# Optimization experiments

Hardware: AMD Instinct MI355X
Metric: run time of the kernel (lower is better)

Reference implementation:

```python
import jax, jax.numpy as jnp
import numpy as np
from jax.ops import segment_sum, segment_max

H, C = 2, 32            # heads, per-head channels (hidden = H*C = 64)
HID = H * C
L = 2                   # num_layers
EPS = 1e-5              # LayerNorm eps
NEG_SLOPE = 0.2         # GATv2 leaky_relu slope
NP_, NA_, E_, DIN, DOUT = 200_000, 100_000, 1_000_000, 128, 64


def setup_inputs() -> dict:
    ks = jax.random.split(jax.random.key(0), 16)
    s = 0.05
    return {
        "x_paper": jax.random.normal(ks[0], (NP_, DIN), jnp.float32),
        "x_author": jax.random.normal(ks[1], (NA_, DIN), jnp.float32),
        "ei_writes_src": jax.random.randint(ks[2], (E_,), 0, NA_),
        "ei_writes_dst": jax.random.randint(ks[3], (E_,), 0, NP_),
        "ei_rev_src": jax.random.randint(ks[4], (E_,), 0, NP_),
        "ei_rev_dst": jax.random.randint(ks[5], (E_,), 0, NA_),
        "ei_cites_src": jax.random.randint(ks[6], (E_,), 0, NP_),
        "ei_cites_dst": jax.random.randint(ks[7], (E_,), 0, NP_),
        "inW_paper": jax.random.normal(ks[8], (DIN, HID)) * s,
        "inW_author": jax.random.normal(ks[9], (DIN, HID)) * s,
        "gat_Wl": jax.random.normal(ks[10], (L, 3, HID, HID)) * s,
        "gat_bl": jnp.zeros((L, 3, HID)),
        "gat_Wr": jax.random.normal(ks[11], (L, 3, HID, HID)) * s,
        "gat_br": jnp.zeros((L, 3, HID)),
        "gat_att": jax.random.normal(ks[12], (L, 3, H, C)) * s,
        "gat_bias": jnp.zeros((L, 3, HID)),
        "ln_scale": jnp.ones((L, 2, HID)),
        "ln_bias": jnp.zeros((L, 2, HID)),
        "outW_paper": jax.random.normal(ks[13], (HID, DOUT)) * s,
        "outb_paper": jnp.zeros((DOUT,)),
        "outW_author": jax.random.normal(ks[14], (HID, DOUT)) * s,
        "outb_author": jnp.zeros((DOUT,)),
    }


def _gatv2(h_src, h_dst, src, dst, Wl, bl, Wr, br, att, bias):
    """PyG GATv2Conv(64, 32, heads=2, concat=True, add_self_loops=False)."""
    nd = h_dst.shape[0]
    xl = (h_src @ Wl + bl).reshape(-1, H, C)           # [Ns,H,C]
    xr = (h_dst @ Wr + br).reshape(-1, H, C)           # [Nd,H,C]
    e = jax.nn.leaky_relu(xl[src] + xr[dst], NEG_SLOPE)  # [E,H,C] gather+add
    logits = jnp.einsum('ehc,hc->eh', e, att)          # [E,H]
    m = jax.lax.stop_gradient(segment_max(logits, dst, num_segments=nd))
    ex = jnp.exp(logits - m[dst])                      # stable segment softmax
    den = segment_sum(ex, dst, num_segments=nd)
    alpha = ex / den[dst]                              # [E,H]
    agg = segment_sum(xl[src] * alpha[..., None], dst, num_segments=nd)
    return agg.reshape(nd, HID) + bias


def _ln(v, g, b):
    mu = v.mean(-1, keepdims=True)
    var = ((v - mu) ** 2).mean(-1, keepdims=True)
    return (v - mu) / jnp.sqrt(var + EPS) * g + b


def _forward(x_paper, x_author, ints, params):
    ws, wd, rs, rd, cs, cd = ints
    (inW_p, inW_a, Wl, bl, Wr, br, att, gbias, lng, lnb,
     oWp, obp, oWa, oba) = params
    h = {"paper": x_paper @ inW_p, "author": x_author @ inW_a}
    rels = [("author", "paper", ws, wd),   # writes
            ("paper", "author", rs, rd),   # rev_writes
            ("paper", "paper", cs, cd)]    # cites
    for l in range(L):
        new = {"paper": 0.0, "author": 0.0}
        for r, (st, dt, src, dst) in enumerate(rels):
            new[dt] = new[dt] + _gatv2(h[st], h[dt], src, dst,
                                       Wl[l, r], bl[l, r], Wr[l, r], br[l, r],
                                       att[l, r], gbias[l, r])
        # HeteroConv(aggr='sum') -> LayerNorm -> ReLU (dropout is eval no-op)
        h = {nt: jax.nn.relu(_ln(new[nt], lng[l, i], lnb[l, i]))
             for i, nt in enumerate(("paper", "author"))}
    out_p = h["paper"] @ oWp + obp
    out_a = h["author"] @ oWa + oba
    return jnp.concatenate([out_p, out_a], axis=0)  # [Np+Na, DOUT]


def reference(x_paper, x_author, ei_writes_src, ei_writes_dst, ei_rev_src,
              ei_rev_dst, ei_cites_src, ei_cites_dst, inW_paper, inW_author,
              gat_Wl, gat_bl, gat_Wr, gat_br, gat_att, gat_bias, ln_scale,
              ln_bias, outW_paper, outb_paper, outW_author, outb_author):
    ints = (ei_writes_src, ei_writes_dst, ei_rev_src, ei_rev_dst,
            ei_cites_src, ei_cites_dst)
    params = (inW_paper, inW_author, gat_Wl, gat_bl, gat_Wr, gat_br, gat_att,
              gat_bias, ln_scale, ln_bias, outW_paper, outb_paper,
              outW_author, outb_author)
    return _forward(x_paper, x_author, ints, params)
```

## Files before the change

### kernel.cpp

```cpp
#include <hip/hip_runtime.h>
#include <hip/hip_bf16.h>


#define NPAPER  200000
#define NAUTHOR 100000
#define NEDGE   1000000

#define NB128_P 1563
#define NB128_A 782

#define BIN_SHIFT 10
#define BIN_SIZE  1024
#define NBIN_P    196
#define NBIN_A    98
#define NBIN_TOT  (NBIN_P + NBIN_A + NBIN_P)
#define CAP_P     8192
#define CAP_A     16384
#define RELOFF1   (NBIN_P * CAP_P)
#define RELOFF2   (NBIN_P * CAP_P + NBIN_A * CAP_A)
#define BINNED_TOT (NBIN_P * CAP_P + NBIN_A * CAP_A + NBIN_P * CAP_P)
#define EPT       8
#define NBLK_BIN  489

#define LOG2E 1.4426950408889634f

typedef __attribute__((ext_vector_type(8))) short short8;
typedef __attribute__((ext_vector_type(4))) float f32x4;
typedef __attribute__((ext_vector_type(2))) float f32x2;

__device__ inline float b2f(__hip_bfloat16 v) { return __bfloat162float(v); }

__device__ inline short f2bs(float f) {
    unsigned u = __float_as_uint(f);
    u += 0x7FFFu + ((u >> 16) & 1u);
    return (short)(u >> 16);
}

__device__ inline float wireF(const void* p, int i, int f32) {
    return f32 ? ((const float*)p)[i]
               : b2f(((const __hip_bfloat16*)p)[i]);
}

__device__ inline const int* sel3(int r, const int* a, const int* b, const int* c) {
    return r == 0 ? a : (r == 1 ? b : c);
}
__device__ inline int* sel3m(int r, int* a, int* b, int* c) {
    return r == 0 ? a : (r == 1 ? b : c);
}

__device__ inline f32x2 unpack2(unsigned u) {
    f32x2 r;
    r.x = __uint_as_float(u << 16);
    r.y = __uint_as_float(u & 0xFFFF0000u);
    return r;
}

template <int CTRL>
__device__ inline float dpp_add(float v) {
    const int r = __builtin_amdgcn_update_dpp(
        0, __float_as_int(v), CTRL, 0xF, 0xF, true);
    return v + __int_as_float(r);
}
__device__ inline float hs16(float v) {
    v = dpp_add<0x128>(v);
    v = dpp_add<0x124>(v);
    v = dpp_add<0x122>(v);
    v = dpp_add<0x121>(v);
    return v;
}
__device__ inline float sum32(float v) {
    v = hs16(v);
    const int s = __builtin_amdgcn_ds_swizzle(__float_as_int(v), 0x401F);
    return v + __int_as_float(s);
}

__global__ void detect_mode(const unsigned* __restrict__ lns, int* __restrict__ flag) {
    if (threadIdx.x == 0 && blockIdx.x == 0)
        flag[0] = (lns[0] == 0x3F800000u) ? 1 : 0;
}

template <int K, int OUT_MODE, bool A_WIRE, bool DBUF>
__global__ __launch_bounds__(256) void gemm_ps(
    const void* __restrict__ A0v, const void* __restrict__ B0v, int b0_off,
    const void* __restrict__ bias0v, int bias0_off,
    void* __restrict__ Y0v, int N0, int row0_off, int nt0, int g0,
    const void* __restrict__ A1v, const void* __restrict__ B1v, int b1_off,
    const void* __restrict__ bias1v, int bias1_off,
    void* __restrict__ Y1v, int N1, int row1_off, int nt1,
    const int* __restrict__ flagp)
{
    const int f32 = flagp[0];
    constexpr int SB = K + 8;
    constexpr int OUTB = (OUT_MODE == 2) ? 8192 : 4096;
    __shared__ short Bs[64 * SB];
    __shared__ float sbias[64];
    __shared__ __align__(16) char outs[4][OUTB];

    int bid = blockIdx.x;
    const void* Av; const void* Bv; int b_off; const void* biasv; int bias_off;
    void* Yv; int N; int row_off; int ntiles; int gstep; int t0;
    if (bid < g0) {
        Av = A0v; Bv = B0v; b_off = b0_off; biasv = bias0v; bias_off = bias0_off;
        Yv = Y0v; N = N0; row_off = row0_off; ntiles = nt0; gstep = g0; t0 = bid;
    } else {
        Av = A1v; Bv = B1v; b_off = b1_off; biasv = bias1v; bias_off = bias1_off;
        Yv = Y1v; N = N1; row_off = row1_off; ntiles = nt1;
        gstep = (int)gridDim.x - g0; t0 = bid - g0;
    }

    const int tid = threadIdx.x;
    for (int idx = tid; idx < K * 64; idx += 256) {
        const int k = idx >> 6;
        const int n = idx & 63;
        const short v = f32 ? f2bs(((const float*)Bv)[b_off + idx])
                            : ((const short*)Bv)[b_off + idx];
        Bs[n * SB + k] = v;
    }
    if (tid < 64)
        sbias[tid] = biasv ? wireF(biasv, bias_off + tid, f32) : 0.0f;
    __syncthreads();

    if (t0 >= ntiles) return;

    const int wave = tid >> 6;
    const int lane = tid & 63;
    const int l15  = lane & 15;
    const int quad = lane >> 4;
    char* const myout = outs[wave];

    short8 a_cur[K / 32][2], a_nxt[K / 32][2];

    auto ldA = [&](int t, short8 (&af)[K / 32][2]) {
        const int rowb = t * 128 + wave * 32;
#pragma unroll
        for (int kit = 0; kit < K / 32; kit++) {
            const int k0 = kit * 32 + quad * 8;
#pragma unroll
            for (int rg = 0; rg < 2; rg++) {
                int r = rowb + rg * 16 + l15;
                if (r >= N) r = N - 1;
                if (A_WIRE && f32) {
                    const float* Ar = (const float*)Av + (size_t)r * K + k0;
                    const float4 x0 = *reinterpret_cast<const float4*>(Ar);
                    const float4 x1 = *reinterpret_cast<const float4*>(Ar + 4);
                    short8 tt;
                    tt[0] = f2bs(x0.x); tt[1] = f2bs(x0.y);
                    tt[2] = f2bs(x0.z); tt[3] = f2bs(x0.w);
                    tt[4] = f2bs(x1.x); tt[5] = f2bs(x1.y);
                    tt[6] = f2bs(x1.z); tt[7] = f2bs(x1.w);
                    af[kit][rg] = tt;
                } else {
                    af[kit][rg] = *reinterpret_cast<const short8*>(
                        (const short*)Av + (size_t)r * K + k0);
                }
            }
        }
    };

    if (DBUF) ldA(t0, a_cur);
    for (int t = t0; ; ) {
        const int tn = t + gstep;
        const bool hn = tn < ntiles;
        if (DBUF) {
            if (hn) ldA(tn, a_nxt);
        } else {
            ldA(t, a_cur);
        }

        f32x4 acc[2][4] = {};
#pragma unroll
        for (int kit = 0; kit < K / 32; kit++) {
            const int k0 = kit * 32 + quad * 8;
#pragma unroll
            for (int cg = 0; cg < 4; cg++) {
                const short8 bf = *reinterpret_cast<const short8*>(
                    &Bs[(cg * 16 + l15) * SB + k0]);
#pragma unroll
                for (int rg = 0; rg < 2; rg++)
                    acc[rg][cg] = __builtin_amdgcn_mfma_f32_16x16x32_bf16(
                        a_cur[kit][rg], bf, acc[rg][cg], 0, 0, 0);
            }
        }

        const int rowbase = t * 128 + wave * 32;
        const bool bf16out = (OUT_MODE == 0) || !f32;
        if (bf16out) {
#pragma unroll
            for (int rg = 0; rg < 2; rg++)
#pragma unroll
            for (int cg = 0; cg < 4; cg++) {
                const int col = cg * 16 + l15;
                const float bv = sbias[col];
#pragma unroll
                for (int r = 0; r < 4; r++) {
                    const int rl = rg * 16 + quad * 4 + r;
                    const unsigned a = (unsigned)(rl * 128 + col * 2)
                                     ^ (unsigned)((rl & 7) << 4);
                    *reinterpret_cast<short*>(myout + a) =
                        f2bs(acc[rg][cg][r] + bv);
                }
            }
#pragma unroll
            for (int i = 0; i < 4; i++) {
                const unsigned a = i * 1024 + lane * 16;
                const int rl = a >> 7;
                const unsigned as = a ^ (unsigned)((rl & 7) << 4);
                const int grow = rowbase + rl;
                if (grow < N) {
                    const uint4 v = *reinterpret_cast<const uint4*>(myout + as);
                    *reinterpret_cast<uint4*>(
                        (__hip_bfloat16*)Yv
                        + (size_t)(grow + row_off) * 64 + ((a & 127) >> 1)) = v;
                }
            }
        } else {
#pragma unroll
            for (int rg = 0; rg < 2; rg++)
#pragma unroll
            for (int cg = 0; cg < 4; cg++) {
                const int col = cg * 16 + l15;
                const float bv = sbias[col];
#pragma unroll
                for (int r = 0; r < 4; r++) {
                    const int rl = rg * 16 + quad * 4 + r;
                    const unsigned a = (unsigned)(rl * 256 + col * 4)
                                     ^ (unsigned)((rl & 15) << 4);
                    *reinterpret_cast<float*>(myout + a) = acc[rg][cg][r] + bv;
                }
            }
#pragma unroll
            for (int i = 0; i < 8; i++) {
                const unsigned a = i * 1024 + lane * 16;
                const int rl = a >> 8;
                const unsigned as = a ^ (unsigned)((rl & 15) << 4);
                const int grow = rowbase + rl;
                if (grow < N) {
                    const float4 v = *reinterpret_cast<const float4*>(myout + as);
                    *reinterpret_cast<float4*>(
                        (float*)Yv
                        + (size_t)(grow + row_off) * 64 + ((a & 255) >> 2)) = v;
                }
            }
        }

        if (!hn) break;
        if (DBUF) {
#pragma unroll
            for (int kit = 0; kit < K / 32; kit++) {
                a_cur[kit][0] = a_nxt[kit][0];
                a_cur[kit][1] = a_nxt[kit][1];
            }
        }
        t = tn;
    }
}

__global__ __launch_bounds__(256) void scatter_pad(
    const int* __restrict__ s0, const int* __restrict__ s1, const int* __restrict__ s2,
    const int* __restrict__ d0, const int* __restrict__ d1, const int* __restrict__ d2,
    int* __restrict__ g_bincnt, unsigned* __restrict__ binned)
{
    int bid = blockIdx.x;
    const int rel = bid / NBLK_BIN;
    bid -= rel * NBLK_BIN;
    const int* src = sel3(rel, s0, s1, s2);
    const int* dst = sel3(rel, d0, d1, d2);
    const int nbin = (rel == 1) ? NBIN_A : NBIN_P;
    const int cap  = (rel == 1) ? CAP_A : CAP_P;
    const int boff = (rel == 0) ? 0 : ((rel == 1) ? NBIN_P : NBIN_P + NBIN_A);
    unsigned* bout = binned + ((rel == 0) ? 0 : ((rel == 1) ? RELOFF1 : RELOFF2));

    __shared__ int lcnt[NBIN_P];
    __shared__ int lbase[NBIN_P];
    for (int i = threadIdx.x; i < nbin; i += 256) lcnt[i] = 0;
    __syncthreads();

    const int e0 = bid * (256 * EPT) + threadIdx.x;
    int mybin[EPT], myslot[EPT];
    unsigned mypack[EPT];
#pragma unroll
    for (int i = 0; i < EPT; i++) {
        const int e = e0 + i * 256;
        if (e < NEDGE) {
            const int D = dst[e];
            const int b = D >> BIN_SHIFT;
            mybin[i]  = b;
            mypack[i] = (unsigned)src[e] | ((unsigned)(D & (BIN_SIZE - 1)) << 18);
            myslot[i] = atomicAdd(&lcnt[b], 1);
        } else mybin[i] = -1;
    }
    __syncthreads();
    for (int i = threadIdx.x; i < nbin; i += 256) {
        const int cn = lcnt[i];
        lbase[i] = cn ? atomicAdd(&g_bincnt[boff + i], cn) : 0;
    }
    __syncthreads();
#pragma unroll
    for (int i = 0; i < EPT; i++)
        if (mybin[i] >= 0) {
            const int pos = lbase[mybin[i]] + myslot[i];
            if (pos < cap)
                bout[(size_t)mybin[i] * cap + pos] = mypack[i];
        }
}

__global__ __launch_bounds__(256) void csr_binscan(
    const int* __restrict__ g_bincnt, int* __restrict__ g_binbase,
    int* __restrict__ rp0, int* __restrict__ rp1, int* __restrict__ rp2)
{
    __shared__ int lds[NBIN_TOT];
    for (int i = threadIdx.x; i < NBIN_TOT; i += 256) lds[i] = g_bincnt[i];
    __syncthreads();
    if (threadIdx.x < 3) {
        const int rel  = threadIdx.x;
        const int nbin = (rel == 1) ? NBIN_A : NBIN_P;
        const int boff = (rel == 0) ? 0 : ((rel == 1) ? NBIN_P : NBIN_P + NBIN_A);
        int run = 0;
        for (int i = 0; i < nbin; i++) {
            const int cn = lds[boff + i];
            lds[boff + i] = run;
            run += cn;
        }
        int* rp = sel3m(rel, rp0, rp1, rp2);
        rp[(rel == 1) ? NAUTHOR : NPAPER] = NEDGE;
    }
    __syncthreads();
    for (int i = threadIdx.x; i < NBIN_TOT; i += 256)
        g_binbase[i] = lds[i];
}

__global__ __launch_bounds__(256) void csr_build(
    const unsigned* __restrict__ binned, const int* __restrict__ g_binbase,
    const int* __restrict__ g_bincnt,
    int* __restrict__ rp0, int* __restrict__ rp1, int* __restrict__ rp2,
    int* __restrict__ c0, int* __restrict__ c1, int* __restrict__ c2)
{
    int bid = blockIdx.x;
    int rel, boff, N, cap;
    const unsigned* bin;
    if (bid < NBIN_P) {
        rel = 0; boff = 0; N = NPAPER; cap = CAP_P;
        bin = binned + (size_t)bid * CAP_P;
    } else if (bid < NBIN_P + NBIN_A) {
        rel = 1; bid -= NBIN_P; boff = NBIN_P; N = NAUTHOR; cap = CAP_A;
        bin = binned + RELOFF1 + (size_t)bid * CAP_A;
    } else {
        rel = 2; bid -= NBIN_P + NBIN_A; boff = NBIN_P + NBIN_A; N = NPAPER; cap = CAP_P;
        bin = binned + RELOFF2 + (size_t)bid * CAP_P;
    }

    const int base = g_binbase[boff + bid];
    int cnt = g_bincnt[boff + bid];
    if (cnt > cap) cnt = cap;
    int* row_ptr = sel3m(rel, rp0, rp1, rp2);
    int* csr     = sel3m(rel, c0, c1, c2);

    __shared__ int off[BIN_SIZE];
    __shared__ int lds[256];
    for (int i = threadIdx.x; i < BIN_SIZE; i += 256) off[i] = 0;
    __syncthreads();
    for (int i = threadIdx.x; i < cnt; i += 256)
        atomicAdd(&off[bin[i] >> 18], 1);
    __syncthreads();

    const int t  = threadIdx.x;
    const int i4 = t * 4;
    const int v0 = off[i4], v1 = off[i4 + 1], v2 = off[i4 + 2], v3 = off[i4 + 3];
    const int tsum = v0 + v1 + v2 + v3;
    lds[t] = tsum;
    __syncthreads();
    for (int o = 1; o < 256; o <<= 1) {
        const int x = (t >= o) ? lds[t - o] : 0;
        __syncthreads();
        lds[t] += x;
        __syncthreads();
    }
    const int run = lds[t] - tsum;
    const int ex0 = run, ex1 = ex0 + v0, ex2 = ex1 + v1, ex3 = ex2 + v2;
    off[i4] = ex0; off[i4 + 1] = ex1; off[i4 + 2] = ex2; off[i4 + 3] = ex3;
    const int d0g = bid * BIN_SIZE + i4;
    if (d0g     < N) row_ptr[d0g]     = base + ex0;
    if (d0g + 1 < N) row_ptr[d0g + 1] = base + ex1;
    if (d0g + 2 < N) row_ptr[d0g + 2] = base + ex2;
    if (d0g + 3 < N) row_ptr[d0g + 3] = base + ex3;
    __syncthreads();

    for (int i = threadIdx.x; i < cnt; i += 256) {
        const unsigned pk = bin[i];
        const int slot = atomicAdd(&off[pk >> 18], 1);
        csr[base + slot] = (int)(pk & 0x3FFFFu);
    }
}

__device__ inline void gat_core_h(
    const int* __restrict__ csr_src, const unsigned* __restrict__ xlw,
    int beg, int end, int hbase, int cp,
    const f32x2 xr2, float a0, float a1,
    float& accx, float& accy, float& den)
{
    const int n = end - beg;
    const int m = (n + 3) >> 2;
    f32x2 acc2 = {0.0f, 0.0f};
    float dn = 0.0f;

    int lidx;
    {
        const int e = beg + cp;
        lidx = csr_src[(e < end) ? e : beg];
    }
    auto loadq = [&](unsigned (&B)[4], int it) {
#pragma unroll
        for (int k = 0; k < 4; k++) {
            const int s = __shfl(lidx, hbase + ((it & 7) << 2) + k, 64);
            B[k] = xlw[(size_t)s * 32 + cp];
        }
    };

    unsigned G[4];
    loadq(G, 0);
    for (int it = 0; ; ) {
        const int nx = it + 1;
        const bool hn = nx < m;
        unsigned H[4];
        if (hn) {
            if ((nx & 7) == 0) {
                const int e = beg + (nx << 2) + cp;
                lidx = csr_src[(e < end) ? e : beg];
            }
            loadq(H, nx);
        }

        f32x2 xv[4];
        float u[4];
#pragma unroll
        for (int k = 0; k < 4; k++) {
            xv[k] = unpack2(G[k]);
            f32x2 t = xv[k] + xr2;
            t = __builtin_elementwise_max(t, 0.2f * t);
            u[k] = fmaf(t.y, a1, t.x * a0);
        }
#pragma unroll
        for (int k = 0; k < 4; k++) u[k] = hs16(u[k]);
#pragma unroll
        for (int k = 0; k < 4; k++) {
            const float e = ((it << 2) + k < n)
                          ? __builtin_amdgcn_exp2f(u[k]) : 0.0f;
            acc2 += e * xv[k];
            dn   += e;
        }

        if (!hn) break;
        G[0] = H[0]; G[1] = H[1]; G[2] = H[2]; G[3] = H[3];
        it = nx;
    }
    accx = acc2.x;
    accy = acc2.y;
    den  = dn;
}

__global__ __launch_bounds__(256) void gat_all(
    const int* __restrict__ rp0, const int* __restrict__ cs0,
    const __hip_bfloat16* __restrict__ xl0, const __hip_bfloat16* __restrict__ xr0,
    const int* __restrict__ rp2, const int* __restrict__ cs2,
    const __hip_bfloat16* __restrict__ xl2, const __hip_bfloat16* __restrict__ xr2,
    const int* __restrict__ rp1, const int* __restrict__ cs1,
    const __hip_bfloat16* __restrict__ xl1, const __hip_bfloat16* __restrict__ xr1,
    const void* __restrict__ att, int ao0, int ao1, int ao2,
    const void* __restrict__ gb, int bo0, int bo1, int bo2,
    const void* __restrict__ lng, int goffP, int goffA,
    const void* __restrict__ lnb, int boffP, int boffA,
    __hip_bfloat16* __restrict__ h_p, __hip_bfloat16* __restrict__ h_a,
    const int* __restrict__ flagp)
{
    const int gnode = blockIdx.x * 8 + (threadIdx.x >> 5);
    const int hbase = threadIdx.x & 32;
    const int cp    = threadIdx.x & 31;
    const int f32   = flagp[0];
    const int c0 = 2 * cp, c1 = 2 * cp + 1;

    float vx, vy;
    const void* lg; const void* lb; int goff, boff;
    __hip_bfloat16* hout; int dout;

    if (gnode < NPAPER) {
        const int d = gnode;
        vx = wireF(gb, bo0 + c0, f32) + wireF(gb, bo2 + c0, f32);
        vy = wireF(gb, bo0 + c1, f32) + wireF(gb, bo2 + c1, f32);

        {
            const int beg = rp0[d], end = rp0[d + 1];
            if (beg != end) {
                const unsigned uxr = ((const unsigned*)xr0)[(size_t)d * 32 + cp];
                float ax, ay, dn;
                gat_core_h(cs0, (const unsigned*)xl0, beg, end, hbase, cp,
                           unpack2(uxr),
                           wireF(att, ao0 + c0, f32) * LOG2E,
                           wireF(att, ao0 + c1, f32) * LOG2E, ax, ay, dn);
                vx += ax / dn; vy += ay / dn;
            }
        }
        {
            const int beg = rp2[d], end = rp2[d + 1];
            if (beg != end) {
                const unsigned uxr = ((const unsigned*)xr2)[(size_t)d * 32 + cp];
                float ax, ay, dn;
                gat_core_h(cs2, (const unsigned*)xl2, beg, end, hbase, cp,
                           unpack2(uxr),
                           wireF(att, ao2 + c0, f32) * LOG2E,
                           wireF(att, ao2 + c1, f32) * LOG2E, ax, ay, dn);
                vx += ax / dn; vy += ay / dn;
            }
        }
        lg = lng; lb = lnb; goff = goffP; boff = boffP;
        hout = h_p; dout = d;
    } else {
        const int d = gnode - NPAPER;
        if (d >= NAUTHOR) return;
        vx = wireF(gb, bo1 + c0, f32);
        vy = wireF(gb, bo1 + c1, f32);

        const int beg = rp1[d], end = rp1[d + 1];
        if (beg != end) {
            const unsigned uxr = ((const unsigned*)xr1)[(size_t)d * 32 + cp];
            float ax, ay, dn;
            gat_core_h(cs1, (const unsigned*)xl1, beg, end, hbase, cp,
                       unpack2(uxr),
                       wireF(att, ao1 + c0, f32) * LOG2E,
                       wireF(att, ao1 + c1, f32) * LOG2E, ax, ay, dn);
            vx += ax / dn; vy += ay / dn;
        }
        lg = lng; lb = lnb; goff = goffA; boff = boffA;
        hout = h_a; dout = d;
    }

    const float mu = sum32(vx + vy) * (1.0f / 64.0f);
    const float dx = vx - mu, dy = vy - mu;
    const float var = sum32(dx * dx + dy * dy) * (1.0f / 64.0f);
    const float sc = rsqrtf(var + 1e-5f);
    float y0 = dx * sc * wireF(lg, goff + c0, f32) + wireF(lb, boff + c0, f32);
    float y1 = dy * sc * wireF(lg, goff + c1, f32) + wireF(lb, boff + c1, f32);
    y0 = (y0 < 0.0f) ? 0.0f : y0;
    y1 = (y1 < 0.0f) ? 0.0f : y1;

    const unsigned u = (unsigned)(unsigned short)f2bs(y0)
                     | ((unsigned)(unsigned short)f2bs(y1) << 16);
    ((unsigned*)hout)[(size_t)dout * 32 + cp] = u;
}

extern "C" void kernel_launch(void* const* d_in, const int* in_sizes, int n_in,
                              void* d_out, int out_size, void* d_ws, size_t ws_size,
                              hipStream_t stream)
{
    const void* x_p   = d_in[0];
    const void* x_a   = d_in[1];
    const int* e_ws_s = (const int*)d_in[2];
    const int* e_ws_d = (const int*)d_in[3];
    const int* e_rv_s = (const int*)d_in[4];
    const int* e_rv_d = (const int*)d_in[5];
    const int* e_ci_s = (const int*)d_in[6];
    const int* e_ci_d = (const int*)d_in[7];
    const void* inW_p = d_in[8];
    const void* inW_a = d_in[9];
    const void* Wl    = d_in[10];
    const void* bl    = d_in[11];
    const void* Wr    = d_in[12];
    const void* br    = d_in[13];
    const void* att   = d_in[14];
    const void* gbias = d_in[15];
    const void* lng   = d_in[16];
    const void* lnb   = d_in[17];
    const void* oWp   = d_in[18];
    const void* obp   = d_in[19];
    const void* oWa   = d_in[20];
    const void* oba   = d_in[21];

    char* p = (char*)d_ws;
    auto carve = [&](size_t bytes) -> char* {
        char* r = p;
        p += (bytes + 255) & ~(size_t)255;
        return r;
    };
    int* flag = (int*)carve(256);
    __hip_bfloat16* h_p = (__hip_bfloat16*)carve((size_t)NPAPER  * 64 * 2);
    __hip_bfloat16* h_a = (__hip_bfloat16*)carve((size_t)NAUTHOR * 64 * 2);
    __hip_bfloat16* xl0 = (__hip_bfloat16*)carve((size_t)NAUTHOR * 64 * 2);
    __hip_bfloat16* xr0 = (__hip_bfloat16*)carve((size_t)NPAPER  * 64 * 2);
    __hip_bfloat16* xl1 = (__hip_bfloat16*)carve((size_t)NPAPER  * 64 * 2);
    __hip_bfloat16* xr1 = (__hip_bfloat16*)carve((size_t)NAUTHOR * 64 * 2);
    __hip_bfloat16* xl2 = (__hip_bfloat16*)carve((size_t)NPAPER  * 64 * 2);
    __hip_bfloat16* xr2 = (__hip_bfloat16*)carve((size_t)NPAPER  * 64 * 2);
    int *csr_src[3], *row_ptr[3];
    for (int r = 0; r < 3; r++) {
        csr_src[r] = (int*)carve((size_t)NEDGE * 4);
        row_ptr[r] = (int*)carve(((size_t)NPAPER + 1) * 4);
    }
    unsigned* binned = (unsigned*)carve((size_t)BINNED_TOT * 4);
    int* g_bincnt  = (int*)carve(NBIN_TOT * 4);
    int* g_binbase = (int*)carve(NBIN_TOT * 4);

    detect_mode<<<dim3(1), dim3(64), 0, stream>>>((const unsigned*)lng, flag);

    (void)hipMemsetAsync(g_bincnt, 0, NBIN_TOT * 4, stream);
    scatter_pad<<<dim3(3 * NBLK_BIN), dim3(256), 0, stream>>>(
        e_ws_s, e_rv_s, e_ci_s, e_ws_d, e_rv_d, e_ci_d, g_bincnt, binned);
    csr_binscan<<<dim3(1), dim3(256), 0, stream>>>(
        g_bincnt, g_binbase, row_ptr[0], row_ptr[1], row_ptr[2]);
    csr_build<<<dim3(NBIN_TOT), dim3(256), 0, stream>>>(
        binned, g_binbase, g_bincnt, row_ptr[0], row_ptr[1], row_ptr[2],
        csr_src[0], csr_src[1], csr_src[2]);

    auto gsplit = [](int GT, int nt0, int nt1) -> int {
        int g0 = (int)((long long)GT * nt0 / (nt0 + nt1));
        if (g0 < 1) g0 = 1;
        if (g0 > GT - 1) g0 = GT - 1;
        return g0;
    };

    {
        const int GT = 1024;
        const int g0 = gsplit(GT, NB128_P, NB128_A);
        gemm_ps<128, 0, true, false><<<dim3(GT), dim3(256), 0, stream>>>(
            x_p, inW_p, 0, nullptr, 0, h_p, NPAPER, 0, NB128_P, g0,
            x_a, inW_a, 0, nullptr, 0, h_a, NAUTHOR, 0, NB128_A, flag);
    }

    for (int l = 0; l < 2; l++) {
        const int wo0 = (l * 3 + 0) * 4096, bo0 = (l * 3 + 0) * 64;
        const int wo1 = (l * 3 + 1) * 4096, bo1 = (l * 3 + 1) * 64;
        const int wo2 = (l * 3 + 2) * 4096, bo2 = (l * 3 + 2) * 64;
        const int GT = 1536;

        {
            const int g0 = gsplit(GT, NB128_A, NB128_P);
            gemm_ps<64, 0, false, true><<<dim3(GT), dim3(256), 0, stream>>>(
                h_a, Wl, wo0, bl, bo0, xl0, NAUTHOR, 0, NB128_A, g0,
                h_p, Wr, wo0, br, bo0, xr0, NPAPER, 0, NB128_P, flag);
        }
        {
            const int g0 = gsplit(GT, NB128_P, NB128_P);
            gemm_ps<64, 0, false, true><<<dim3(GT), dim3(256), 0, stream>>>(
                h_p, Wl, wo2, bl, bo2, xl2, NPAPER, 0, NB128_P, g0,
                h_p, Wr, wo2, br, bo2, xr2, NPAPER, 0, NB128_P, flag);
        }
        {
            const int g0 = gsplit(GT, NB128_P, NB128_A);
            gemm_ps<64, 0, false, true><<<dim3(GT), dim3(256), 0, stream>>>(
                h_p, Wl, wo1, bl, bo1, xl1, NPAPER, 0, NB128_P, g0,
                h_a, Wr, wo1, br, bo1, xr1, NAUTHOR, 0, NB128_A, flag);
        }

        gat_all<<<dim3((NPAPER + NAUTHOR) / 8), dim3(256), 0, stream>>>(
            row_ptr[0], csr_src[0], xl0, xr0,
            row_ptr[2], csr_src[2], xl2, xr2,
            row_ptr[1], csr_src[1], xl1, xr1,
            att, bo0, bo1, bo2,
            gbias, bo0, bo1, bo2,
            lng, (l * 2 + 0) * 64, (l * 2 + 1) * 64,
            lnb, (l * 2 + 0) * 64, (l * 2 + 1) * 64,
            h_p, h_a, flag);
    }

    {
        const int GT = 768;
        const int g0 = gsplit(GT, NB128_P, NB128_A);
        gemm_ps<64, 2, false, true><<<dim3(GT), dim3(256), 0, stream>>>(
            h_p, oWp, 0, obp, 0, d_out, NPAPER, 0, NB128_P, g0,
            h_a, oWa, 0, oba, 0, d_out, NAUTHOR, NPAPER, NB128_A, flag);
    }
}
```

Before: 788.7 us.

## Merge per-layer projection GEMMs into one six-job launch; specialize input/output GEMMs

Replaces the three two-job projection GEMM launches per layer with a single launch that covers all six Wl/Wr projections. A block picks its job from a boundary table passed in a struct. The input projection becomes a dedicated kernel with 64-row tiles, no LDS staging and direct scalar bf16 stores, launched on a larger grid. The output GEMM becomes its own specialized kernel. The aim is to cut launch count and tail effects, at the cost of scalar uncoalesced stores in the input GEMM and a per-block job lookup.

```diff
diff --git a/kernel.cpp b/kernel.cpp
--- a/kernel.cpp
+++ b/kernel.cpp
@@ -8,6 +8,8 @@
 
 #define NB128_P 1563
 #define NB128_A 782
+#define NB64_P  3125
+#define NB64_A  1563
 
 #define BIN_SHIFT 10
 #define BIN_SIZE  1024
@@ -79,47 +81,140 @@
         flag[0] = (lns[0] == 0x3F800000u) ? 1 : 0;
 }
 
-template <int K, int OUT_MODE, bool A_WIRE, bool DBUF>
-__global__ __launch_bounds__(256) void gemm_ps(
-    const void* __restrict__ A0v, const void* __restrict__ B0v, int b0_off,
-    const void* __restrict__ bias0v, int bias0_off,
-    void* __restrict__ Y0v, int N0, int row0_off, int nt0, int g0,
-    const void* __restrict__ A1v, const void* __restrict__ B1v, int b1_off,
-    const void* __restrict__ bias1v, int bias1_off,
-    void* __restrict__ Y1v, int N1, int row1_off, int nt1,
+__global__ __launch_bounds__(256) void gemm_in(
+    const void* __restrict__ A0v, const void* __restrict__ B0v,
+    void* __restrict__ Y0v, int N0, int nt0, int g0,
+    const void* __restrict__ A1v, const void* __restrict__ B1v,
+    void* __restrict__ Y1v, int N1, int nt1,
     const int* __restrict__ flagp)
 {
     const int f32 = flagp[0];
-    constexpr int SB = K + 8;
-    constexpr int OUTB = (OUT_MODE == 2) ? 8192 : 4096;
+    constexpr int K = 128, SB = K + 8;
+    __shared__ short Bs[64 * SB];
+
+    int bid = blockIdx.x;
+    const void* Av; const void* Bv; void* Yv; int N, ntiles, gstep, t0;
+    if (bid < g0) {
+        Av = A0v; Bv = B0v; Yv = Y0v; N = N0; ntiles = nt0; gstep = g0; t0 = bid;
+    } else {
+        Av = A1v; Bv = B1v; Yv = Y1v; N = N1; ntiles = nt1;
+        gstep = (int)gridDim.x - g0; t0 = bid - g0;
+    }
+
+    const int tid = threadIdx.x;
+    for (int idx = tid; idx < K * 64; idx += 256) {
+        const int k = idx >> 6, n = idx & 63;
+        const short v = f32 ? f2bs(((const float*)Bv)[idx])
+                            : ((const short*)Bv)[idx];
+        Bs[n * SB + k] = v;
+    }
+    __syncthreads();
+    if (t0 >= ntiles) return;
+
+    const int wave = tid >> 6;
+    const int lane = tid & 63;
+    const int l15  = lane & 15;
+    const int quad = lane >> 4;
+
+    for (int t = t0; t < ntiles; t += gstep) {
+        const int rowbase = t * 64 + wave * 16;
+        int r = rowbase + l15;
+        if (r >= N) r = N - 1;
+
+        short8 af[4];
+#pragma unroll
+        for (int kit = 0; kit < 4; kit++) {
+            const int k0 = kit * 32 + quad * 8;
+            if (f32) {
+                const float* Ar = (const float*)Av + (size_t)r * K + k0;
+                const float4 x0 = *reinterpret_cast<const float4*>(Ar);
+                const float4 x1 = *reinterpret_cast<const float4*>(Ar + 4);
+                short8 tt;
+                tt[0] = f2bs(x0.x); tt[1] = f2bs(x0.y);
+                tt[2] = f2bs(x0.z); tt[3] = f2bs(x0.w);
+                tt[4] = f2bs(x1.x); tt[5] = f2bs(x1.y);
+                tt[6] = f2bs(x1.z); tt[7] = f2bs(x1.w);
+                af[kit] = tt;
+            } else {
+                af[kit] = *reinterpret_cast<const short8*>(
+                    (const short*)Av + (size_t)r * K + k0);
+            }
+        }
+
+        f32x4 acc[4] = {};
+#pragma unroll
+        for (int kit = 0; kit < 4; kit++) {
+            const int k0 = kit * 32 + quad * 8;
+#pragma unroll
+            for (int cg = 0; cg < 4; cg++) {
+                const short8 bf = *reinterpret_cast<const short8*>(
+                    &Bs[(cg * 16 + l15) * SB + k0]);
+                acc[cg] = __builtin_amdgcn_mfma_f32_16x16x32_bf16(
+                    af[kit], bf, acc[cg], 0, 0, 0);
+            }
+        }
+
+#pragma unroll
+        for (int cg = 0; cg < 4; cg++) {
+            const int col = cg * 16 + l15;
+#pragma unroll
+            for (int rr = 0; rr < 4; rr++) {
+                const int row = rowbase + quad * 4 + rr;
+                if (row < N)
+                    ((__hip_bfloat16*)Yv)[(size_t)row * 64 + col] =
+                        __float2bfloat16(acc[cg][rr]);
+            }
+        }
+    }
+}
+
+struct J6 {
+    const void* A[6];
+    const void* W[6];
+    int         woff[6];
+    const void* bias[6];
+    int         boff[6];
+    void*       Y[6];
+    int         N[6];
+    int         nt[6];
+    int         gb[7];
+};
+
+__global__ __launch_bounds__(256) void gemm_ps6(J6 j, const int* __restrict__ flagp)
+{
+    const int f32 = flagp[0];
+    constexpr int K = 64, SB = K + 8;
     __shared__ short Bs[64 * SB];
     __shared__ float sbias[64];
-    __shared__ __align__(16) char outs[4][OUTB];
-
-    int bid = blockIdx.x;
-    const void* Av; const void* Bv; int b_off; const void* biasv; int bias_off;
-    void* Yv; int N; int row_off; int ntiles; int gstep; int t0;
-    if (bid < g0) {
-        Av = A0v; Bv = B0v; b_off = b0_off; biasv = bias0v; bias_off = bias0_off;
-        Yv = Y0v; N = N0; row_off = row0_off; ntiles = nt0; gstep = g0; t0 = bid;
-    } else {
-        Av = A1v; Bv = B1v; b_off = b1_off; biasv = bias1v; bias_off = bias1_off;
-        Yv = Y1v; N = N1; row_off = row1_off; ntiles = nt1;
-        gstep = (int)gridDim.x - g0; t0 = bid - g0;
-    }
+    __shared__ __align__(16) char outs[4][4096];
+
+    const int bid = blockIdx.x;
+    int jid = 0;
+#pragma unroll
+    for (int q = 0; q < 5; q++)
+        if (bid >= j.gb[q + 1]) jid = q + 1;
+
+    const void* Av = j.A[jid];
+    void* Yv = j.Y[jid];
+    const int N = j.N[jid];
+    const int ntiles = j.nt[jid];
+    const int gstep = j.gb[jid + 1] - j.gb[jid];
+    const int t0 = bid - j.gb[jid];
 
     const int tid = threadIdx.x;
-    for (int idx = tid; idx < K * 64; idx += 256) {
-        const int k = idx >> 6;
-        const int n = idx & 63;
-        const short v = f32 ? f2bs(((const float*)Bv)[b_off + idx])
-                            : ((const short*)Bv)[b_off + idx];
-        Bs[n * SB + k] = v;
-    }
-    if (tid < 64)
-        sbias[tid] = biasv ? wireF(biasv, bias_off + tid, f32) : 0.0f;
-    __syncthreads();
-
+    {
+        const short* Ws = (const short*)j.W[jid];
+        const float* Wf = (const float*)j.W[jid];
+        const int wo = j.woff[jid];
+        for (int idx = tid; idx < K * 64; idx += 256) {
+            const int k = idx >> 6, n = idx & 63;
+            const short v = f32 ? f2bs(Wf[wo + idx]) : Ws[wo + idx];
+            Bs[n * SB + k] = v;
+        }
+        if (tid < 64)
+            sbias[tid] = wireF(j.bias[jid], j.boff[jid] + tid, f32);
+    }
+    __syncthreads();
     if (t0 >= ntiles) return;
 
     const int wave = tid >> 6;
@@ -128,48 +223,32 @@
     const int quad = lane >> 4;
     char* const myout = outs[wave];
 
-    short8 a_cur[K / 32][2], a_nxt[K / 32][2];
-
-    auto ldA = [&](int t, short8 (&af)[K / 32][2]) {
+    short8 a_cur[2][2], a_nxt[2][2];
+
+    auto ldA = [&](int t, short8 (&af)[2][2]) {
         const int rowb = t * 128 + wave * 32;
 #pragma unroll
-        for (int kit = 0; kit < K / 32; kit++) {
+        for (int kit = 0; kit < 2; kit++) {
             const int k0 = kit * 32 + quad * 8;
 #pragma unroll
             for (int rg = 0; rg < 2; rg++) {
                 int r = rowb + rg * 16 + l15;
                 if (r >= N) r = N - 1;
-                if (A_WIRE && f32) {
-                    const float* Ar = (const float*)Av + (size_t)r * K + k0;
-                    const float4 x0 = *reinterpret_cast<const float4*>(Ar);
-                    const float4 x1 = *reinterpret_cast<const float4*>(Ar + 4);
-                    short8 tt;
-                    tt[0] = f2bs(x0.x); tt[1] = f2bs(x0.y);
-                    tt[2] = f2bs(x0.z); tt[3] = f2bs(x0.w);
-                    tt[4] = f2bs(x1.x); tt[5] = f2bs(x1.y);
-                    tt[6] = f2bs(x1.z); tt[7] = f2bs(x1.w);
-                    af[kit][rg] = tt;
-                } else {
-                    af[kit][rg] = *reinterpret_cast<const short8*>(
-                        (const short*)Av + (size_t)r * K + k0);
-                }
+                af[kit][rg] = *reinterpret_cast<const short8*>(
+                    (const short*)Av + (size_t)r * K + k0);
             }
         }
     };
 
-    if (DBUF) ldA(t0, a_cur);
+    ldA(t0, a_cur);
     for (int t = t0; ; ) {
         const int tn = t + gstep;
         const bool hn = tn < ntiles;
-        if (DBUF) {
-            if (hn) ldA(tn, a_nxt);
-        } else {
-            ldA(t, a_cur);
-        }
+        if (hn) ldA(tn, a_nxt);
 
         f32x4 acc[2][4] = {};
 #pragma unroll
-        for (int kit = 0; kit < K / 32; kit++) {
+        for (int kit = 0; kit < 2; kit++) {
             const int k0 = kit * 32 + quad * 8;
 #pragma unroll
             for (int cg = 0; cg < 4; cg++) {
@@ -183,8 +262,125 @@
         }
 
         const int rowbase = t * 128 + wave * 32;
-        const bool bf16out = (OUT_MODE == 0) || !f32;
-        if (bf16out) {
+#pragma unroll
+        for (int rg = 0; rg < 2; rg++)
+#pragma unroll
+        for (int cg = 0; cg < 4; cg++) {
+            const int col = cg * 16 + l15;
+            const float bv = sbias[col];
+#pragma unroll
+            for (int r = 0; r < 4; r++) {
+                const int rl = rg * 16 + quad * 4 + r;
+                const unsigned a = (unsigned)(rl * 128 + col * 2)
+                                 ^ (unsigned)((rl & 7) << 4);
+                *reinterpret_cast<short*>(myout + a) =
+                    f2bs(acc[rg][cg][r] + bv);
+            }
+        }
+#pragma unroll
+        for (int i = 0; i < 4; i++) {
+            const unsigned a = i * 1024 + lane * 16;
+            const int rl = a >> 7;
+            const unsigned as = a ^ (unsigned)((rl & 7) << 4);
+            const int grow = rowbase + rl;
+            if (grow < N) {
+                const uint4 v = *reinterpret_cast<const uint4*>(myout + as);
+                *reinterpret_cast<uint4*>(
+                    (__hip_bfloat16*)Yv + (size_t)grow * 64 + ((a & 127) >> 1)) = v;
+            }
+        }
+
+        if (!hn) break;
+#pragma unroll
+        for (int kit = 0; kit < 2; kit++) {
+            a_cur[kit][0] = a_nxt[kit][0];
+            a_cur[kit][1] = a_nxt[kit][1];
+        }
+        t = tn;
+    }
+}
+
+__global__ __launch_bounds__(256) void gemm_out(
+    const void* __restrict__ A0v, const void* __restrict__ B0v,
+    const void* __restrict__ bias0v,
+    void* __restrict__ Yv, int N0, int row0_off, int nt0, int g0,
+    const void* __restrict__ A1v, const void* __restrict__ B1v,
+    const void* __restrict__ bias1v, int N1, int row1_off, int nt1,
+    const int* __restrict__ flagp)
+{
+    const int f32 = flagp[0];
+    constexpr int K = 64, SB = K + 8;
+    __shared__ short Bs[64 * SB];
+    __shared__ float sbias[64];
+    __shared__ __align__(16) char outs[4][8192];
+
+    int bid = blockIdx.x;
+    const void* Av; const void* Bv; const void* biasv;
+    int N, row_off, ntiles, gstep, t0;
+    if (bid < g0) {
+        Av = A0v; Bv = B0v; biasv = bias0v; N = N0; row_off = row0_off;
+        ntiles = nt0; gstep = g0; t0 = bid;
+    } else {
+        Av = A1v; Bv = B1v; biasv = bias1v; N = N1; row_off = row1_off;
+        ntiles = nt1; gstep = (int)gridDim.x - g0; t0 = bid - g0;
+    }
+
+    const int tid = threadIdx.x;
+    for (int idx = tid; idx < K * 64; idx += 256) {
+        const int k = idx >> 6, n = idx & 63;
+        const short v = f32 ? f2bs(((const float*)Bv)[idx])
+                            : ((const short*)Bv)[idx];
+        Bs[n * SB + k] = v;
+    }
+    if (tid < 64) sbias[tid] = wireF(biasv, tid, f32);
+    __syncthreads();
+    if (t0 >= ntiles) return;
+
+    const int wave = tid >> 6;
+    const int lane = tid & 63;
+    const int l15  = lane & 15;
+    const int quad = lane >> 4;
+    char* const myout = outs[wave];
+
+    short8 a_cur[2][2], a_nxt[2][2];
+    auto ldA = [&](int t, short8 (&af)[2][2]) {
+        const int rowb = t * 128 + wave * 32;
+#pragma unroll
+        for (int kit = 0; kit < 2; kit++) {
+            const int k0 = kit * 32 + quad * 8;
+#pragma unroll
+            for (int rg = 0; rg < 2; rg++) {
+                int r = rowb + rg * 16 + l15;
+                if (r >= N) r = N - 1;
+                af[kit][rg] = *reinterpret_cast<const short8*>(
+                    (const short*)Av + (size_t)r * K + k0);
+            }
+        }
+    };
+
+    ldA(t0, a_cur);
+    for (int t = t0; ; ) {
+        const int tn = t + gstep;
+        const bool hn = tn < ntiles;
+        if (hn) ldA(tn, a_nxt);
+
+        f32x4 acc[2][4] = {};
+#pragma unroll
+        for (int kit = 0; kit < 2; kit++) {
+            const int k0 = kit * 32 + quad * 8;
+#pragma unroll
+            for (int cg = 0; cg < 4; cg++) {
+                const short8 bf = *reinterpret_cast<const short8*>(
+                    &Bs[(cg * 16 + l15) * SB + k0]);
+#pragma unroll
+                for (int rg = 0; rg < 2; rg++)
+                    acc[rg][cg] = __builtin_amdgcn_mfma_f32_16x16x32_bf16(
+                        a_cur[kit][rg], bf, acc[rg][cg], 0, 0, 0);
+            }
+        }
+
+        const int rowbase = t * 128 + wave * 32;
+        if (!f32) {
 #pragma unroll
             for (int rg = 0; rg < 2; rg++)
 #pragma unroll
@@ -244,12 +440,10 @@
         }
 
         if (!hn) break;
-        if (DBUF) {
-#pragma unroll
-            for (int kit = 0; kit < K / 32; kit++) {
-                a_cur[kit][0] = a_nxt[kit][0];
-                a_cur[kit][1] = a_nxt[kit][1];
-            }
+#pragma unroll
+        for (int kit = 0; kit < 2; kit++) {
+            a_cur[kit][0] = a_nxt[kit][0];
+            a_cur[kit][1] = a_nxt[kit][1];
         }
         t = tn;
     }
@@ -479,7 +673,7 @@
     const int c0 = 2 * cp, c1 = 2 * cp + 1;
 
     float vx, vy;
-    const void* lg; const void* lb; int goff, boff;
+    int goff, boff;
     __hip_bfloat16* hout; int dout;
 
     if (gnode < NPAPER) {
@@ -511,7 +705,7 @@
                 vx += ax / dn; vy += ay / dn;
             }
         }
-        lg = lng; lb = lnb; goff = goffP; boff = boffP;
+        goff = goffP; boff = boffP;
         hout = h_p; dout = d;
     } else {
         const int d = gnode - NPAPER;
@@ -529,7 +723,7 @@
                        wireF(att, ao1 + c1, f32) * LOG2E, ax, ay, dn);
             vx += ax / dn; vy += ay / dn;
         }
-        lg = lng; lb = lnb; goff = goffA; boff = boffA;
+        goff = goffA; boff = boffA;
         hout = h_a; dout = d;
     }
 
@@ -537,8 +731,8 @@
     const float dx = vx - mu, dy = vy - mu;
     const float var = sum32(dx * dx + dy * dy) * (1.0f / 64.0f);
     const float sc = rsqrtf(var + 1e-5f);
-    float y0 = dx * sc * wireF(lg, goff + c0, f32) + wireF(lb, boff + c0, f32);
-    float y1 = dy * sc * wireF(lg, goff + c1, f32) + wireF(lb, boff + c1, f32);
+    float y0 = dx * sc * wireF(lng, goff + c0, f32) + wireF(lnb, boff + c0, f32);
+    float y1 = dy * sc * wireF(lng, goff + c1, f32) + wireF(lnb, boff + c1, f32);
     y0 = (y0 < 0.0f) ? 0.0f : y0;
     y1 = (y1 < 0.0f) ? 0.0f : y1;
 
@@ -609,45 +803,42 @@
         binned, g_binbase, g_bincnt, row_ptr[0], row_ptr[1], row_ptr[2],
         csr_src[0], csr_src[1], csr_src[2]);
 
-    auto gsplit = [](int GT, int nt0, int nt1) -> int {
-        int g0 = (int)((long long)GT * nt0 / (nt0 + nt1));
-        if (g0 < 1) g0 = 1;
-        if (g0 > GT - 1) g0 = GT - 1;
-        return g0;
-    };
-
     {
-        const int GT = 1024;
-        const int g0 = gsplit(GT, NB128_P, NB128_A);
-        gemm_ps<128, 0, true, false><<<dim3(GT), dim3(256), 0, stream>>>(
-            x_p, inW_p, 0, nullptr, 0, h_p, NPAPER, 0, NB128_P, g0,
-            x_a, inW_a, 0, nullptr, 0, h_a, NAUTHOR, 0, NB128_A, flag);
+        const int GT = 2048;
+        const int g0 = (int)((long long)GT * NB64_P / (NB64_P + NB64_A));
+        gemm_in<<<dim3(GT), dim3(256), 0, stream>>>(
+            x_p, inW_p, h_p, NPAPER, NB64_P, g0,
+            x_a, inW_a, h_a, NAUTHOR, NB64_A, flag);
     }
 
     for (int l = 0; l < 2; l++) {
         const int wo0 = (l * 3 + 0) * 4096, bo0 = (l * 3 + 0) * 64;
         const int wo1 = (l * 3 + 1) * 4096, bo1 = (l * 3 + 1) * 64;
         const int wo2 = (l * 3 + 2) * 4096, bo2 = (l * 3 + 2) * 64;
-        const int GT = 1536;
-
-        {
-            const int g0 = gsplit(GT, NB128_A, NB128_P);
-            gemm_ps<64, 0, false, true><<<dim3(GT), dim3(256), 0, stream>>>(
-                h_a, Wl, wo0, bl, bo0, xl0, NAUTHOR, 0, NB128_A, g0,
-                h_p, Wr, wo0, br, bo0, xr0, NPAPER, 0, NB128_P, flag);
-        }
-        {
-            const int g0 = gsplit(GT, NB128_P, NB128_P);
-            gemm_ps<64, 0, false, true><<<dim3(GT), dim3(256), 0, stream>>>(
-                h_p, Wl, wo2, bl, bo2, xl2, NPAPER, 0, NB128_P, g0,
-                h_p, Wr, wo2, br, bo2, xr2, NPAPER, 0, NB128_P, flag);
-        }
-        {
-            const int g0 = gsplit(GT, NB128_P, NB128_A);
-            gemm_ps<64, 0, false, true><<<dim3(GT), dim3(256), 0, stream>>>(
-                h_p, Wl, wo1, bl, bo1, xl1, NPAPER, 0, NB128_P, g0,
-                h_a, Wr, wo1, br, bo1, xr1, NAUTHOR, 0, NB128_A, flag);
-        }
+
+        J6 j;
+        const void* As[6] = { h_a, h_p, h_p, h_p, h_p, h_a };
+        const void* Ws[6] = { Wl,  Wr,  Wl,  Wr,  Wl,  Wr  };
+        const int  wos[6] = { wo0, wo0, wo2, wo2, wo1, wo1 };
+        const void* Bi[6] = { bl,  br,  bl,  br,  bl,  br  };
+        const int  bos[6] = { bo0, bo0, bo2, bo2, bo1, bo1 };
+        void*      Ys[6] = { xl0, xr0, xl2, xr2, xl1, xr1 };
+        const int  Nsz[6] = { NAUTHOR, NPAPER, NPAPER, NPAPER, NPAPER, NAUTHOR };
+        const int  nts[6] = { NB128_A, NB128_P, NB128_P, NB128_P, NB128_P, NB128_A };
+        const int GT6 = 1536;
+        int total = 0;
+        for (int q = 0; q < 6; q++) total += nts[q];
+        j.gb[0] = 0;
+        for (int q = 0; q < 6; q++) {
+            j.A[q] = As[q]; j.W[q] = Ws[q]; j.woff[q] = wos[q];
+            j.bias[q] = Bi[q]; j.boff[q] = bos[q];
+            j.Y[q] = Ys[q]; j.N[q] = Nsz[q]; j.nt[q] = nts[q];
+            int g = (int)((long long)GT6 * nts[q] / total);
+            if (g < 1) g = 1;
+            j.gb[q + 1] = j.gb[q] + g;
+        }
+        j.gb[6] = GT6;
+        gemm_ps6<<<dim3(GT6), dim3(256), 0, stream>>>(j, flag);
 
         gat_all<<<dim3((NPAPER + NAUTHOR) / 8), dim3(256), 0, stream>>>(
             row_ptr[0], csr_src[0], xl0, xr0,
@@ -662,9 +853,9 @@
 
     {
         const int GT = 768;
-        const int g0 = gsplit(GT, NB128_P, NB128_A);
-        gemm_ps<64, 2, false, true><<<dim3(GT), dim3(256), 0, stream>>>(
-            h_p, oWp, 0, obp, 0, d_out, NPAPER, 0, NB128_P, g0,
-            h_a, oWa, 0, oba, 0, d_out, NAUTHOR, NPAPER, NB128_A, flag);
-    }
-}
+        const int g0 = (int)((long long)GT * NB128_P / (NB128_P + NB128_A));
+        gemm_out<<<dim3(GT), dim3(256), 0, stream>>>(
+            h_p, oWp, obp, d_out, NPAPER, 0, NB128_P, g0,
+            h_a, oWa, oba, NAUTHOR, NPAPER, NB128_A, flag);
+    }
+}
```

After: 724.3 us (median of 2 runs). 8.2% less time.
